# Kernel tuning notes

Hardware: AMD Instinct MI355X
Metric: run time of the kernel (lower is better)

## Reference

```python
import jax, jax.numpy as jnp
import numpy as np

D = 128   # node feature dim
C = 2     # classes
N = 50000 # nodes
E = 500000  # edges (before self-loops)
H1 = 2    # conv1 heads
NEG_SLOPE = 0.2
BN_EPS = 1e-5


def setup_inputs() -> dict:
    key = jax.random.key(0)
    ks = jax.random.split(key, 24)
    rn = lambda k, shape, s=0.05: jax.random.normal(k, shape, dtype=jnp.float32) * s
    inp = {
        'x': jax.random.normal(ks[0], (N, D), dtype=jnp.float32),
        'edge_index': jax.random.randint(ks[1], (2, E), 0, N, dtype=jnp.int64),
        # conv1: GATConv(D, D, heads=2, concat=True)
        'W1': rn(ks[2], (D, H1 * D)),
        'att_src1': rn(ks[3], (H1, D)),
        'att_dst1': rn(ks[4], (H1, D)),
        'bias1': jnp.zeros((H1 * D,), jnp.float32),
        # conv2: GATConv(2D, D, heads=1, concat=False)
        'W2': rn(ks[5], (2 * D, D)),
        'att_src2': rn(ks[6], (1, D)),
        'att_dst2': rn(ks[7], (1, D)),
        'bias2': jnp.zeros((D,), jnp.float32),
        # lin1 = MLP([3D, 96]) : Linear -> ReLU -> BatchNorm1d
        'Wl': rn(ks[8], (3 * D, 96)), 'bl': jnp.zeros((96,), jnp.float32),
        'gl': jnp.ones((96,), jnp.float32), 'betal': jnp.zeros((96,), jnp.float32),
        # mlp1 = MLP([96, 96, C]) : two (Linear -> ReLU -> BN) blocks
        'Wa': rn(ks[9], (96, 96)), 'ba': jnp.zeros((96,), jnp.float32),
        'ga': jnp.ones((96,), jnp.float32), 'betaa': jnp.zeros((96,), jnp.float32),
        'Wb': rn(ks[10], (96, C)), 'bb': jnp.zeros((C,), jnp.float32),
        'gb': jnp.ones((C,), jnp.float32), 'betab': jnp.zeros((C,), jnp.float32),
    }
    return inp


def gat_conv(x, src, dst, W, att_src, att_dst, bias, heads, out_dim, concat):
    # PyG GATConv: h = x W -> [N,H,F]; per-edge logit leakyrelu(a_s.h_src + a_d.h_dst);
    # segment softmax over edges grouped by destination; weighted scatter-sum.
    n = x.shape[0]
    h = (x @ W).reshape(n, heads, out_dim)
    a_src = jnp.einsum('nhd,hd->nh', h, att_src)  # [N,H]
    a_dst = jnp.einsum('nhd,hd->nh', h, att_dst)
    alpha = jax.nn.leaky_relu(a_src[src] + a_dst[dst], NEG_SLOPE)  # [Etot,H]
    m = jax.ops.segment_max(alpha, dst, num_segments=n)            # [N,H]
    e = jnp.exp(alpha - m[dst])
    s = jax.ops.segment_sum(e, dst, num_segments=n)
    w = e / (s[dst] + 1e-16)                                       # [Etot,H]
    out = jax.ops.segment_sum(h[src] * w[:, :, None], dst, num_segments=n)  # [N,H,F]
    out = out.reshape(n, heads * out_dim) if concat else out.mean(axis=1)
    return out + bias


def mlp_block(x, W, b, gamma, beta):
    # Linear -> ReLU -> BatchNorm1d (training-mode batch stats, biased var)
    y = jax.nn.relu(x @ W + b)
    mu = y.mean(axis=0)
    var = ((y - mu) ** 2).mean(axis=0)
    return gamma * (y - mu) / jnp.sqrt(var + BN_EPS) + beta


def reference(x, edge_index, W1, att_src1, att_dst1, bias1,
              W2, att_src2, att_dst2, bias2,
              Wl, bl, gl, betal, Wa, ba, ga, betaa, Wb, bb, gb, betab):
    n = x.shape[0]
    # PyG GATConv default add_self_loops=True
    loops = jnp.arange(n, dtype=edge_index.dtype)
    src = jnp.concatenate([edge_index[0], loops])
    dst = jnp.concatenate([edge_index[1], loops])
    x1 = gat_conv(x, src, dst, W1, att_src1, att_dst1, bias1, H1, D, True)    # [N,2D]
    x2 = gat_conv(x1, src, dst, W2, att_src2, att_dst2, bias2, 1, D, False)   # [N,D]
    h = jnp.concatenate([x1, x2], axis=1)                                      # [N,3D]
    h = mlp_block(h, Wl, bl, gl, betal)     # lin1
    h = mlp_block(h, Wa, ba, ga, betaa)     # mlp1 layer 1
    h = mlp_block(h, Wb, bb, gb, betab)     # mlp1 layer 2
    return h
```

## Files before the change

kernel.cpp:

```cpp
#include <hip/hip_runtime.h>
#include <hip/hip_bf16.h>
#include <cstdint>
#include <cstddef>

#define NNODES 50000
#define NEDGES 500000
#define ETOT   (NEDGES + NNODES)
#define MAXDEG 96

typedef __attribute__((ext_vector_type(8))) short short8;
typedef __attribute__((ext_vector_type(8))) unsigned short ushort8v;
typedef __attribute__((ext_vector_type(4))) float floatx4;
typedef __attribute__((ext_vector_type(4))) unsigned short ushort4v;

__device__ __forceinline__ unsigned short f2bf(float f) {
    union { __hip_bfloat16 h; unsigned short u; } cv;
    cv.h = __float2bfloat16(f);
    return cv.u;
}
__device__ __forceinline__ float bf2f(unsigned short u) {
    union { unsigned int i; float f; } cv;
    cv.i = ((unsigned int)u) << 16;
    return cv.f;
}

#define GBM 128
#define GBN 64
#define GBK 32

__global__ __launch_bounds__(256, 4) void gemm_mfma(
    const unsigned short* __restrict__ A, int lda,
    const unsigned short* __restrict__ Bt,
    float* __restrict__ C,
    unsigned short* __restrict__ Cb,
    const float* __restrict__ bias,
    float* __restrict__ colsum, float* __restrict__ colsq,
    const float* __restrict__ att_s, const float* __restrict__ att_d,
    float* __restrict__ as_out, float* __restrict__ ad_out, int Hheads,
    int M, int N, int K, int do_relu)
{
    __shared__ __attribute__((aligned(16))) unsigned short Alds[GBM * GBK];
    __shared__ __attribute__((aligned(16))) unsigned short Blds[GBN * GBK];
    __shared__ float scol[GBN], sqcol[GBN];

    int tid = threadIdx.x;
    int wave = tid >> 6, lane = tid & 63;
    int row0 = blockIdx.y * GBM;
    int col0 = blockIdx.x * GBN;
    int m = lane & 15, q = lane >> 4;

    floatx4 acc[2][4] = {};

    for (int k0 = 0; k0 < K; k0 += GBK) {
        #pragma unroll
        for (int i = 0; i < 2; ++i) {
            int c = tid + i * 256;
            int r = c >> 2, off = (c & 3) * 8;
            int gr = row0 + r;
            short8 v = {};
            if (gr < M) v = *(const short8*)(A + (size_t)gr * lda + k0 + off);
            *(short8*)(Alds + r * GBK + off) = v;
        }
        {
            int r = tid >> 2, off = (tid & 3) * 8;
            short8 v = *(const short8*)(Bt + (size_t)(col0 + r) * K + k0 + off);
            *(short8*)(Blds + r * GBK + off) = v;
        }
        __syncthreads();

        short8 a0 = *(const short8*)(Alds + (wave * 32 + m) * GBK + q * 8);
        short8 a1 = *(const short8*)(Alds + (wave * 32 + 16 + m) * GBK + q * 8);
        #pragma unroll
        for (int ct = 0; ct < 4; ++ct) {
            short8 b = *(const short8*)(Blds + (ct * 16 + m) * GBK + q * 8);
            acc[0][ct] = __builtin_amdgcn_mfma_f32_16x16x32_bf16(a0, b, acc[0][ct], 0, 0, 0);
            acc[1][ct] = __builtin_amdgcn_mfma_f32_16x16x32_bf16(a1, b, acc[1][ct], 0, 0, 0);
        }
        __syncthreads();
    }

    float ps[4] = {}, pq[4] = {};
    #pragma unroll
    for (int rt = 0; rt < 2; ++rt) {
        #pragma unroll
        for (int r = 0; r < 4; ++r) {
            int gr = row0 + wave * 32 + rt * 16 + q * 4 + r;
            float ds = 0.f, dd = 0.f;
            #pragma unroll
            for (int ct = 0; ct < 4; ++ct) {
                int gc = col0 + ct * 16 + m;
                float v = acc[rt][ct][r];
                if (gc < N) {
                    if (att_s != nullptr) { ds += v * att_s[gc]; dd += v * att_d[gc]; }
                    float vb = v;
                    if (bias != nullptr) vb += bias[gc];
                    if (do_relu) vb = fmaxf(vb, 0.f);
                    if (gr < M) {
                        if (C  != nullptr) C[(size_t)gr * N + gc] = vb;
                        if (Cb != nullptr) Cb[(size_t)gr * N + gc] = f2bf(vb);
                        ps[ct] += vb; pq[ct] += vb * vb;
                    }
                }
            }
            if (att_s != nullptr) {
                #pragma unroll
                for (int off = 1; off < 16; off <<= 1) {
                    ds += __shfl_xor(ds, off);
                    dd += __shfl_xor(dd, off);
                }
                if (m == 0 && gr < M) {
                    int head = col0 >> 7;
                    atomicAdd(&as_out[gr * Hheads + head], ds);
                    atomicAdd(&ad_out[gr * Hheads + head], dd);
                }
            }
        }
    }
    if (colsum != nullptr) {
        if (tid < GBN) { scol[tid] = 0.f; sqcol[tid] = 0.f; }
        __syncthreads();
        #pragma unroll
        for (int ct = 0; ct < 4; ++ct) {
            atomicAdd(&scol[ct * 16 + m], ps[ct]);
            atomicAdd(&sqcol[ct * 16 + m], pq[ct]);
        }
        __syncthreads();
        if (tid < GBN) {
            int gc = col0 + tid;
            if (gc < N) {
                atomicAdd(&colsum[gc], scol[tid]);
                atomicAdd(&colsq[gc], sqcol[tid]);
            }
        }
    }
}

__global__ void cast_x_k(const float* __restrict__ x, unsigned short* __restrict__ xb, int total4) {
    int i = blockIdx.x * blockDim.x + threadIdx.x;
    if (i >= total4) return;
    const float4 v = ((const float4*)x)[i];
    ushort4v o;
    o.x = f2bf(v.x); o.y = f2bf(v.y); o.z = f2bf(v.z); o.w = f2bf(v.w);
    ((ushort4v*)xb)[i] = o;
}

__global__ void cast_weights(const float* __restrict__ W1, const float* __restrict__ W2,
                             const float* __restrict__ Wl,
                             unsigned short* __restrict__ W1t, unsigned short* __restrict__ W2t,
                             unsigned short* __restrict__ Wlt) {
    int i = blockIdx.x * 256 + threadIdx.x;
    if (i < 32768) {
        int n = i >> 7, k = i & 127;
        W1t[i] = f2bf(W1[k * 256 + n]);
    } else if (i < 65536) {
        int j = i - 32768;
        int n = j >> 8, k = j & 255;
        W2t[j] = f2bf(W2[k * 128 + n]);
    } else if (i < 114688) {
        int j = i - 65536;
        int n = j / 384, k = j % 384;
        Wlt[j] = (n < 96) ? f2bf(Wl[(size_t)k * 96 + n]) : (unsigned short)0;
    }
}

__global__ void bnfold_a(const float* __restrict__ csum, const float* __restrict__ csq,
                         const float* __restrict__ gamma, const float* __restrict__ beta,
                         const float* __restrict__ Wa, const float* __restrict__ ba,
                         unsigned short* __restrict__ Wat2, float* __restrict__ ba_f) {
    __shared__ float scl[96], shf[96];
    int tid = threadIdx.x;
    if (tid < 96) {
        float mu  = csum[tid] / (float)NNODES;
        float var = csq[tid] / (float)NNODES - mu * mu;
        if (var < 0.f) var = 0.f;
        float sc = gamma[tid] * rsqrtf(var + 1e-5f);
        scl[tid] = sc; shf[tid] = beta[tid] - mu * sc;
    }
    __syncthreads();
    for (int idx = tid; idx < 128 * 96; idx += 256) {
        int n = idx / 96, k = idx % 96;
        Wat2[idx] = (n < 96) ? f2bf(scl[k] * Wa[k * 96 + n]) : (unsigned short)0;
    }
    if (tid < 96) {
        float s = ba[tid];
        for (int k = 0; k < 96; ++k) s += shf[k] * Wa[k * 96 + tid];
        ba_f[tid] = s;
    }
}

__global__ void bnfold_b(const float* __restrict__ csum, const float* __restrict__ csq,
                         const float* __restrict__ gamma, const float* __restrict__ beta,
                         const float* __restrict__ Wb, const float* __restrict__ bb,
                         unsigned short* __restrict__ Wbt, float* __restrict__ bb_f) {
    __shared__ float scl[96], shf[96];
    int tid = threadIdx.x;
    if (tid < 96) {
        float mu  = csum[tid] / (float)NNODES;
        float var = csq[tid] / (float)NNODES - mu * mu;
        if (var < 0.f) var = 0.f;
        float sc = gamma[tid] * rsqrtf(var + 1e-5f);
        scl[tid] = sc; shf[tid] = beta[tid] - mu * sc;
    }
    __syncthreads();
    for (int idx = tid; idx < 64 * 96; idx += 256) {
        int n = idx / 96, k = idx % 96;
        Wbt[idx] = (n < 2) ? f2bf(scl[k] * Wb[k * 2 + n]) : (unsigned short)0;
    }
    if (tid < 2) {
        float s = bb[tid];
        for (int k = 0; k < 96; ++k) s += shf[k] * Wb[k * 2 + tid];
        bb_f[tid] = s;
    }
}

__global__ void bn_fin_apply(const float* __restrict__ csum, const float* __restrict__ csq,
                             const float* __restrict__ gamma, const float* __restrict__ beta,
                             float* __restrict__ y, int total) {
    int i = blockIdx.x * blockDim.x + threadIdx.x;
    if (i >= total) return;
    int j = i & 1;
    float mu  = csum[j] / (float)NNODES;
    float var = csq[j] / (float)NNODES - mu * mu;
    if (var < 0.f) var = 0.f;
    float sc = gamma[j] * rsqrtf(var + 1e-5f);
    float sh = beta[j] - mu * sc;
    y[i] = y[i] * sc + sh;
}

__device__ __forceinline__ void edge_src_dst(const int* ei, int e, int& src, int& dst) {
    if (e < NEDGES) { src = ei[e]; dst = ei[NEDGES + e]; }
    else { src = e - NEDGES; dst = src; }
}

__global__ __launch_bounds__(256) void csr_count(const int* __restrict__ ei, int* __restrict__ cnt) {
    int e = blockIdx.x * blockDim.x + threadIdx.x;
    if (e >= ETOT) return;
    int src, dst; edge_src_dst(ei, e, src, dst); (void)src;
    atomicAdd(&cnt[dst], 1);
}

#define SCAN_CH 1024
#define SCAN_NB ((NNODES + SCAN_CH - 1) / SCAN_CH)

__global__ __launch_bounds__(256) void scan1(const int* __restrict__ cnt, int* __restrict__ part) {
    int t = threadIdx.x;
    int base = blockIdx.x * SCAN_CH + t * 4;
    int4 v = {0, 0, 0, 0};
    if (base + 3 < NNODES) v = *(const int4*)(cnt + base);
    else {
        if (base + 0 < NNODES) v.x = cnt[base + 0];
        if (base + 1 < NNODES) v.y = cnt[base + 1];
        if (base + 2 < NNODES) v.z = cnt[base + 2];
        if (base + 3 < NNODES) v.w = cnt[base + 3];
    }
    int s = v.x + v.y + v.z + v.w;
    __shared__ int sm[256];
    sm[t] = s;
    __syncthreads();
    for (int off = 128; off > 0; off >>= 1) {
        if (t < off) sm[t] += sm[t + off];
        __syncthreads();
    }
    if (t == 0) part[blockIdx.x] = sm[0];
}

__global__ void scan2(int* __restrict__ part, int* __restrict__ rowstart) {
    int lane = threadIdx.x;
    int v = (lane < SCAN_NB) ? part[lane] : 0;
    #pragma unroll
    for (int off = 1; off < 64; off <<= 1) {
        int t = __shfl_up(v, off);
        if (lane >= off) v += t;
    }
    int ex = __shfl_up(v, 1);
    if (lane == 0) ex = 0;
    if (lane < SCAN_NB) part[lane] = ex;
    if (lane == 0) rowstart[NNODES] = ETOT;
}

__global__ __launch_bounds__(256) void scan3(const int* __restrict__ cnt, const int* __restrict__ part,
                                             int* __restrict__ rowstart, int* __restrict__ cursor) {
    int t = threadIdx.x;
    int base = blockIdx.x * SCAN_CH + t * 4;
    int4 v = {0, 0, 0, 0};
    if (base + 3 < NNODES) v = *(const int4*)(cnt + base);
    else {
        if (base + 0 < NNODES) v.x = cnt[base + 0];
        if (base + 1 < NNODES) v.y = cnt[base + 1];
        if (base + 2 < NNODES) v.z = cnt[base + 2];
        if (base + 3 < NNODES) v.w = cnt[base + 3];
    }
    int s = v.x + v.y + v.z + v.w;
    __shared__ int sm[2][256];
    sm[0][t] = s;
    __syncthreads();
    int cur = 0;
    #pragma unroll
    for (int off = 1; off < 256; off <<= 1) {
        int nxt = cur ^ 1;
        int val = sm[cur][t];
        if (t >= off) val += sm[cur][t - off];
        sm[nxt][t] = val;
        __syncthreads();
        cur = nxt;
    }
    int p = sm[cur][t] - s + part[blockIdx.x];
    if (base + 0 < NNODES) { rowstart[base + 0] = p; cursor[base + 0] = p; } p += v.x;
    if (base + 1 < NNODES) { rowstart[base + 1] = p; cursor[base + 1] = p; } p += v.y;
    if (base + 2 < NNODES) { rowstart[base + 2] = p; cursor[base + 2] = p; } p += v.z;
    if (base + 3 < NNODES) { rowstart[base + 3] = p; cursor[base + 3] = p; }
}

__global__ __launch_bounds__(256) void csr_fill(const int* __restrict__ ei,
                                                int* __restrict__ cursor,
                                                int* __restrict__ esrc) {
    int e = blockIdx.x * blockDim.x + threadIdx.x;
    if (e >= ETOT) return;
    int src, dst; edge_src_dst(ei, e, src, dst);
    int pos = atomicAdd(&cursor[dst], 1);
    esrc[pos] = src;
}

__global__ __launch_bounds__(256) void gat_gather_h2(
    const int* __restrict__ rowstart, const int* __restrict__ esrc,
    const unsigned short* __restrict__ hb, const float* __restrict__ a_src,
    const float* __restrict__ a_dst, const float* __restrict__ bias,
    unsigned short* __restrict__ xcat)
{
    __shared__ float wl[4][2][MAXDEG];
    __shared__ int   esl[4][MAXDEG];
    int wave = threadIdx.x >> 6;
    int n = (blockIdx.x * blockDim.x + threadIdx.x) >> 6;
    int lane = threadIdx.x & 63;
    if (n >= NNODES) return;
    int beg = rowstart[n], end = rowstart[n + 1];
    int deg = end - beg;
    float ad0 = a_dst[n * 2], ad1 = a_dst[n * 2 + 1];

    float m0 = -1e30f, m1 = -1e30f;
    for (int idx = lane; idx < deg; idx += 64) {
        int s = esrc[beg + idx];
        float l0 = a_src[s * 2] + ad0;     l0 = l0 >= 0.f ? l0 : 0.2f * l0;
        float l1 = a_src[s * 2 + 1] + ad1; l1 = l1 >= 0.f ? l1 : 0.2f * l1;
        m0 = fmaxf(m0, l0); m1 = fmaxf(m1, l1);
        if (idx < MAXDEG) { wl[wave][0][idx] = l0; wl[wave][1][idx] = l1; esl[wave][idx] = s; }
    }
    #pragma unroll
    for (int off = 1; off < 64; off <<= 1) {
        m0 = fmaxf(m0, __shfl_xor(m0, off));
        m1 = fmaxf(m1, __shfl_xor(m1, off));
    }
    float s0 = 0.f, s1 = 0.f;
    for (int idx = lane; idx < deg; idx += 64) {
        float l0, l1;
        if (idx < MAXDEG) { l0 = wl[wave][0][idx]; l1 = wl[wave][1][idx]; }
        else {
            int s = esrc[beg + idx];
            l0 = a_src[s * 2] + ad0;     l0 = l0 >= 0.f ? l0 : 0.2f * l0;
            l1 = a_src[s * 2 + 1] + ad1; l1 = l1 >= 0.f ? l1 : 0.2f * l1;
        }
        float e0 = __expf(l0 - m0), e1 = __expf(l1 - m1);
        s0 += e0; s1 += e1;
        if (idx < MAXDEG) { wl[wave][0][idx] = e0; wl[wave][1][idx] = e1; }
    }
    #pragma unroll
    for (int off = 1; off < 64; off <<= 1) {
        s0 += __shfl_xor(s0, off);
        s1 += __shfl_xor(s1, off);
    }

    int g  = lane >> 5;
    int sl = lane & 31;
    int head = sl >> 4;
    float mh   = head ? m1 : m0;
    float invh = head ? 1.f / (s1 + 1e-16f) : 1.f / (s0 + 1e-16f);
    float adh  = head ? ad1 : ad0;

    float acc[8] = {}, acc2[8] = {};
    for (int idx = g; idx < deg; idx += 4) {
        int sA; float wA;
        if (idx < MAXDEG) { sA = esl[wave][idx]; wA = wl[wave][head][idx] * invh; }
        else {
            sA = esrc[beg + idx];
            float l = a_src[sA * 2 + head] + adh; l = l >= 0.f ? l : 0.2f * l;
            wA = __expf(l - mh) * invh;
        }
        const ushort8v hvA = *(const ushort8v*)(hb + (size_t)sA * 256 + sl * 8);
        int i2 = idx + 2;
        if (i2 < deg) {
            int sB; float wB;
            if (i2 < MAXDEG) { sB = esl[wave][i2]; wB = wl[wave][head][i2] * invh; }
            else {
                sB = esrc[beg + i2];
                float l = a_src[sB * 2 + head] + adh; l = l >= 0.f ? l : 0.2f * l;
                wB = __expf(l - mh) * invh;
            }
            const ushort8v hvB = *(const ushort8v*)(hb + (size_t)sB * 256 + sl * 8);
            #pragma unroll
            for (int j = 0; j < 8; ++j) acc2[j] += wB * bf2f(hvB[j]);
        }
        #pragma unroll
        for (int j = 0; j < 8; ++j) acc[j] += wA * bf2f(hvA[j]);
    }
    #pragma unroll
    for (int j = 0; j < 8; ++j) acc[j] += acc2[j];
    #pragma unroll
    for (int j = 0; j < 8; ++j) acc[j] += __shfl_xor(acc[j], 32);
    if (g == 0) {
        ushort8v o;
        #pragma unroll
        for (int j = 0; j < 8; ++j) o[j] = f2bf(acc[j] + bias[sl * 8 + j]);
        *(ushort8v*)(xcat + (size_t)n * 384 + sl * 8) = o;
    }
}

__global__ __launch_bounds__(256) void gat_gather_h1(
    const int* __restrict__ rowstart, const int* __restrict__ esrc,
    const unsigned short* __restrict__ hb, const float* __restrict__ a_src,
    const float* __restrict__ a_dst, const float* __restrict__ bias,
    unsigned short* __restrict__ xcat)
{
    __shared__ float wl[4][MAXDEG];
    __shared__ int   esl[4][MAXDEG];
    int wave = threadIdx.x >> 6;
    int n = (blockIdx.x * blockDim.x + threadIdx.x) >> 6;
    int lane = threadIdx.x & 63;
    if (n >= NNODES) return;
    int beg = rowstart[n], end = rowstart[n + 1];
    int deg = end - beg;
    float ad0 = a_dst[n];

    float m0 = -1e30f;
    for (int idx = lane; idx < deg; idx += 64) {
        int s = esrc[beg + idx];
        float l0 = a_src[s] + ad0; l0 = l0 >= 0.f ? l0 : 0.2f * l0;
        m0 = fmaxf(m0, l0);
        if (idx < MAXDEG) { wl[wave][idx] = l0; esl[wave][idx] = s; }
    }
    #pragma unroll
    for (int off = 1; off < 64; off <<= 1) m0 = fmaxf(m0, __shfl_xor(m0, off));
    float s0 = 0.f;
    for (int idx = lane; idx < deg; idx += 64) {
        float l0;
        if (idx < MAXDEG) l0 = wl[wave][idx];
        else {
            int s = esrc[beg + idx];
            l0 = a_src[s] + ad0; l0 = l0 >= 0.f ? l0 : 0.2f * l0;
        }
        float e0 = __expf(l0 - m0);
        s0 += e0;
        if (idx < MAXDEG) wl[wave][idx] = e0;
    }
    #pragma unroll
    for (int off = 1; off < 64; off <<= 1) s0 += __shfl_xor(s0, off);
    float inv0 = 1.f / (s0 + 1e-16f);

    int g  = lane >> 4;
    int sl = lane & 15;

    float acc[8] = {}, acc2[8] = {};
    for (int idx = g; idx < deg; idx += 8) {
        int sA; float wA;
        if (idx < MAXDEG) { sA = esl[wave][idx]; wA = wl[wave][idx] * inv0; }
        else {
            sA = esrc[beg + idx];
            float l = a_src[sA] + ad0; l = l >= 0.f ? l : 0.2f * l;
            wA = __expf(l - m0) * inv0;
        }
        const ushort8v hvA = *(const ushort8v*)(hb + (size_t)sA * 128 + sl * 8);
        int i2 = idx + 4;
        if (i2 < deg) {
            int sB; float wB;
            if (i2 < MAXDEG) { sB = esl[wave][i2]; wB = wl[wave][i2] * inv0; }
            else {
                sB = esrc[beg + i2];
                float l = a_src[sB] + ad0; l = l >= 0.f ? l : 0.2f * l;
                wB = __expf(l - m0) * inv0;
            }
            const ushort8v hvB = *(const ushort8v*)(hb + (size_t)sB * 128 + sl * 8);
            #pragma unroll
            for (int j = 0; j < 8; ++j) acc2[j] += wB * bf2f(hvB[j]);
        }
        #pragma unroll
        for (int j = 0; j < 8; ++j) acc[j] += wA * bf2f(hvA[j]);
    }
    #pragma unroll
    for (int j = 0; j < 8; ++j) acc[j] += acc2[j];
    #pragma unroll
    for (int j = 0; j < 8; ++j) acc[j] += __shfl_xor(acc[j], 16);
    #pragma unroll
    for (int j = 0; j < 8; ++j) acc[j] += __shfl_xor(acc[j], 32);
    if (g == 0) {
        ushort8v o;
        #pragma unroll
        for (int j = 0; j < 8; ++j) o[j] = f2bf(acc[j] + bias[sl * 8 + j]);
        *(ushort8v*)(xcat + (size_t)n * 384 + 256 + sl * 8) = o;
    }
}

extern "C" void kernel_launch(void* const* d_in, const int* in_sizes, int n_in,
                              void* d_out, int out_size, void* d_ws, size_t ws_size,
                              hipStream_t stream) {
    const float* x        = (const float*)d_in[0];
    const int*   ei       = (const int*)d_in[1];
    const float* W1       = (const float*)d_in[2];
    const float* att_src1 = (const float*)d_in[3];
    const float* att_dst1 = (const float*)d_in[4];
    const float* bias1    = (const float*)d_in[5];
    const float* W2       = (const float*)d_in[6];
    const float* att_src2 = (const float*)d_in[7];
    const float* att_dst2 = (const float*)d_in[8];
    const float* bias2    = (const float*)d_in[9];
    const float* Wl       = (const float*)d_in[10];
    const float* bl       = (const float*)d_in[11];
    const float* gl       = (const float*)d_in[12];
    const float* betal    = (const float*)d_in[13];
    const float* Wa       = (const float*)d_in[14];
    const float* ba       = (const float*)d_in[15];
    const float* ga       = (const float*)d_in[16];
    const float* betaa    = (const float*)d_in[17];
    const float* Wb       = (const float*)d_in[18];
    const float* bb       = (const float*)d_in[19];
    const float* gb       = (const float*)d_in[20];
    const float* betab    = (const float*)d_in[21];
    float* out = (float*)d_out;
    char* ws = (char*)d_ws;

    const int N = NNODES;

    const size_t offY2b  = 0;
    const size_t offXcat = 19200000;
    const size_t offXb   = 57600000;
    const size_t offY1b  = 70400000;
    const size_t offHb1  = 80000000;
    const size_t offW1t  = 105600000;
    const size_t offW2t  = 105665536;
    const size_t offWlt  = 105731072;
    const size_t offWat2 = 105829376;
    const size_t offWbt  = 105853952;
    const size_t offBaf  = 105866240;
    const size_t offBbf  = 105866640;
    const size_t offRow  = 106000000;
    const size_t offCur  = 106200128;
    const size_t offEsrc = 106400832;
    const size_t offPart = 108700000;
    const size_t offAs1  = 108800000;
    const size_t offAd1  = 109200000;
    const size_t offAs2  = 109600000;
    const size_t offAd2  = 109800000;
    const size_t offSt   = 110000000;

    unsigned short* y2b  = (unsigned short*)(ws + offY2b);
    unsigned short* xcat = (unsigned short*)(ws + offXcat);
    unsigned short* xb   = (unsigned short*)(ws + offXb);
    unsigned short* hb2  = (unsigned short*)(ws + offXb);
    unsigned short* y1b  = (unsigned short*)(ws + offY1b);
    unsigned short* hb1  = (unsigned short*)(ws + offHb1);
    unsigned short* W1t  = (unsigned short*)(ws + offW1t);
    unsigned short* W2t  = (unsigned short*)(ws + offW2t);
    unsigned short* Wlt  = (unsigned short*)(ws + offWlt);
    unsigned short* Wat2 = (unsigned short*)(ws + offWat2);
    unsigned short* Wbt  = (unsigned short*)(ws + offWbt);
    float* ba_f = (float*)(ws + offBaf);
    float* bb_f = (float*)(ws + offBbf);
    int* rowst  = (int*)(ws + offRow);
    int* cursor = (int*)(ws + offCur);
    int* esrc   = (int*)(ws + offEsrc);
    int* part   = (int*)(ws + offPart);
    float* as1  = (float*)(ws + offAs1);
    float* ad1  = (float*)(ws + offAd1);
    float* as2  = (float*)(ws + offAs2);
    float* ad2  = (float*)(ws + offAd2);

    float* csum_l = (float*)(ws + offSt + 0);
    float* csq_l  = (float*)(ws + offSt + 512);
    float* csum_a = (float*)(ws + offSt + 2048);
    float* csq_a  = (float*)(ws + offSt + 2560);
    float* csum_b = (float*)(ws + offSt + 4096);
    float* csq_b  = (float*)(ws + offSt + 4608);

    hipMemsetAsync(ws + offRow, 0, (NNODES + 1) * sizeof(int), stream);
    hipMemsetAsync(ws + offAs1, 0, (offSt + 6144) - offAs1, stream);

    dim3 blk(256);
    int edgeBlocks  = (ETOT + 255) / 256;
    int waveBlocksN = (N + 3) / 4;

    cast_x_k<<<(N * 128 / 4 + 255) / 256, blk, 0, stream>>>(x, xb, N * 128 / 4);
    cast_weights<<<(114688 + 255) / 256, blk, 0, stream>>>(W1, W2, Wl, W1t, W2t, Wlt);

    csr_count<<<edgeBlocks, blk, 0, stream>>>(ei, rowst);
    scan1<<<SCAN_NB, blk, 0, stream>>>(rowst, part);
    scan2<<<1, 64, 0, stream>>>(part, rowst);
    scan3<<<SCAN_NB, blk, 0, stream>>>(rowst, part, rowst, cursor);
    csr_fill<<<edgeBlocks, blk, 0, stream>>>(ei, cursor, esrc);

    gemm_mfma<<<dim3(4, (N + GBM - 1) / GBM), blk, 0, stream>>>(
        xb, 128, W1t, nullptr, hb1, nullptr, nullptr, nullptr,
        att_src1, att_dst1, as1, ad1, 2, N, 256, 128, 0);
    gat_gather_h2<<<waveBlocksN, blk, 0, stream>>>(rowst, esrc, hb1, as1, ad1, bias1, xcat);

    gemm_mfma<<<dim3(2, (N + GBM - 1) / GBM), blk, 0, stream>>>(
        xcat, 384, W2t, nullptr, hb2, nullptr, nullptr, nullptr,
        att_src2, att_dst2, as2, ad2, 1, N, 128, 256, 0);
    gat_gather_h1<<<waveBlocksN, blk, 0, stream>>>(rowst, esrc, hb2, as2, ad2, bias2, xcat);

    gemm_mfma<<<dim3(2, (N + GBM - 1) / GBM), blk, 0, stream>>>(
        xcat, 384, Wlt, nullptr, y1b, bl, csum_l, csq_l,
        nullptr, nullptr, nullptr, nullptr, 0, N, 96, 384, 1);
    bnfold_a<<<1, 256, 0, stream>>>(csum_l, csq_l, gl, betal, Wa, ba, Wat2, ba_f);

    gemm_mfma<<<dim3(2, (N + GBM - 1) / GBM), blk, 0, stream>>>(
        y1b, 96, Wat2, nullptr, y2b, ba_f, csum_a, csq_a,
        nullptr, nullptr, nullptr, nullptr, 0, N, 96, 96, 1);
    bnfold_b<<<1, 256, 0, stream>>>(csum_a, csq_a, ga, betaa, Wb, bb, Wbt, bb_f);

    gemm_mfma<<<dim3(1, (N + GBM - 1) / GBM), blk, 0, stream>>>(
        y2b, 96, Wbt, out, nullptr, bb_f, csum_b, csq_b,
        nullptr, nullptr, nullptr, nullptr, 0, N, 2, 96, 1);

    bn_fin_apply<<<(N * 2 + 255) / 256, blk, 0, stream>>>(csum_b, csq_b, gb, betab, out, N * 2);
}
```

Before: 400.8 us.

## Aggregate raw features before conv1 projection and fold attention vectors into weights

Conv1 now gathers neighbours of the 128-wide bf16 input x with per-head softmax weights, then applies W1 per head with two GEMMs. Before, the 256-wide projected h was gathered. Attention logits for conv1 come from precomputed U1 = W1·att vectors, applied in the cast kernel. Conv2 logits come from U2 folded into the first-layer GEMM epilogue, which now applies them after bias. The goal is to halve gather bytes per edge and drop the first full projection GEMM, at the cost of two per-head GEMMs and extra small kernels.

```diff
diff --git a/kernel.cpp b/kernel.cpp
--- a/kernel.cpp
+++ b/kernel.cpp
@@ -32,7 +32,7 @@
     const unsigned short* __restrict__ A, int lda,
     const unsigned short* __restrict__ Bt,
     float* __restrict__ C,
-    unsigned short* __restrict__ Cb,
+    unsigned short* __restrict__ Cb, int ldc,
     const float* __restrict__ bias,
     float* __restrict__ colsum, float* __restrict__ colsq,
     const float* __restrict__ att_s, const float* __restrict__ att_d,
@@ -91,13 +91,13 @@
                 int gc = col0 + ct * 16 + m;
                 float v = acc[rt][ct][r];
                 if (gc < N) {
-                    if (att_s != nullptr) { ds += v * att_s[gc]; dd += v * att_d[gc]; }
                     float vb = v;
                     if (bias != nullptr) vb += bias[gc];
                     if (do_relu) vb = fmaxf(vb, 0.f);
+                    if (att_s != nullptr) { ds += vb * att_s[gc]; dd += vb * att_d[gc]; }
                     if (gr < M) {
-                        if (C  != nullptr) C[(size_t)gr * N + gc] = vb;
-                        if (Cb != nullptr) Cb[(size_t)gr * N + gc] = f2bf(vb);
+                        if (C  != nullptr) C[(size_t)gr * ldc + gc] = vb;
+                        if (Cb != nullptr) Cb[(size_t)gr * ldc + gc] = f2bf(vb);
                         ps[ct] += vb; pq[ct] += vb * vb;
                     }
                 }
@@ -135,13 +135,77 @@
     }
 }
 
-__global__ void cast_x_k(const float* __restrict__ x, unsigned short* __restrict__ xb, int total4) {
-    int i = blockIdx.x * blockDim.x + threadIdx.x;
-    if (i >= total4) return;
-    const float4 v = ((const float4*)x)[i];
+__global__ __launch_bounds__(256) void fold_att(
+    const float* __restrict__ W1, const float* __restrict__ as1v, const float* __restrict__ ad1v,
+    const float* __restrict__ W2, const float* __restrict__ as2v, const float* __restrict__ ad2v,
+    float* __restrict__ U1, float* __restrict__ U2)
+{
+    int g = threadIdx.x >> 5, l = threadIdx.x & 31;
+    int task = blockIdx.x * 8 + g;
+    float ss = 0.f, sd = 0.f;
+    if (task < 256) {
+        int d = task & 127, h = task >> 7;
+        const float4 wv = *(const float4*)(W1 + d * 256 + h * 128 + l * 4);
+        const float4 av = *(const float4*)(as1v + h * 128 + l * 4);
+        const float4 bv = *(const float4*)(ad1v + h * 128 + l * 4);
+        ss = wv.x * av.x + wv.y * av.y + wv.z * av.z + wv.w * av.w;
+        sd = wv.x * bv.x + wv.y * bv.y + wv.z * bv.z + wv.w * bv.w;
+    } else {
+        int k = task - 256;
+        const float4 wv = *(const float4*)(W2 + (size_t)k * 128 + l * 4);
+        const float4 av = *(const float4*)(as2v + l * 4);
+        const float4 bv = *(const float4*)(ad2v + l * 4);
+        ss = wv.x * av.x + wv.y * av.y + wv.z * av.z + wv.w * av.w;
+        sd = wv.x * bv.x + wv.y * bv.y + wv.z * bv.z + wv.w * bv.w;
+    }
+    #pragma unroll
+    for (int off = 1; off < 32; off <<= 1) { ss += __shfl_xor(ss, off); sd += __shfl_xor(sd, off); }
+    if (l == 0) {
+        if (task < 256) {
+            int d = task & 127, h = task >> 7;
+            U1[h * 128 + d] = ss;
+            U1[256 + h * 128 + d] = sd;
+        } else {
+            int k = task - 256;
+            U2[k] = ss;
+            U2[256 + k] = sd;
+        }
+    }
+}
+
+__global__ __launch_bounds__(256) void cast_x_att(
+    const float* __restrict__ x, const float* __restrict__ U1,
+    unsigned short* __restrict__ xb, float* __restrict__ as1, float* __restrict__ ad1)
+{
+    __shared__ float Us[512];
+    int tid = threadIdx.x;
+    Us[tid] = U1[tid];
+    Us[tid + 256] = U1[tid + 256];
+    __syncthreads();
+    int g = tid >> 5, l = tid & 31;
+    int n = blockIdx.x * 8 + g;
+    if (n >= NNODES) return;
+    const float4 v = *(const float4*)(x + (size_t)n * 128 + l * 4);
     ushort4v o;
     o.x = f2bf(v.x); o.y = f2bf(v.y); o.z = f2bf(v.z); o.w = f2bf(v.w);
-    ((ushort4v*)xb)[i] = o;
+    *(ushort4v*)(xb + (size_t)n * 128 + l * 4) = o;
+    const float4 us0 = *(const float4*)(Us + l * 4);
+    const float4 us1 = *(const float4*)(Us + 128 + l * 4);
+    const float4 ud0 = *(const float4*)(Us + 256 + l * 4);
+    const float4 ud1 = *(const float4*)(Us + 384 + l * 4);
+    float s0 = v.x * us0.x + v.y * us0.y + v.z * us0.z + v.w * us0.w;
+    float s1 = v.x * us1.x + v.y * us1.y + v.z * us1.z + v.w * us1.w;
+    float d0 = v.x * ud0.x + v.y * ud0.y + v.z * ud0.z + v.w * ud0.w;
+    float d1 = v.x * ud1.x + v.y * ud1.y + v.z * ud1.z + v.w * ud1.w;
+    #pragma unroll
+    for (int off = 1; off < 32; off <<= 1) {
+        s0 += __shfl_xor(s0, off); s1 += __shfl_xor(s1, off);
+        d0 += __shfl_xor(d0, off); d1 += __shfl_xor(d1, off);
+    }
+    if (l == 0) {
+        as1[n * 2] = s0; as1[n * 2 + 1] = s1;
+        ad1[n * 2] = d0; ad1[n * 2 + 1] = d1;
+    }
 }
 
 __global__ void cast_weights(const float* __restrict__ W1, const float* __restrict__ W2,
@@ -321,11 +385,10 @@
     esrc[pos] = src;
 }
 
-__global__ __launch_bounds__(256) void gat_gather_h2(
+__global__ __launch_bounds__(256) void gat_gather_x2(
     const int* __restrict__ rowstart, const int* __restrict__ esrc,
-    const unsigned short* __restrict__ hb, const float* __restrict__ a_src,
-    const float* __restrict__ a_dst, const float* __restrict__ bias,
-    unsigned short* __restrict__ xcat)
+    const unsigned short* __restrict__ xb, const float* __restrict__ a_src,
+    const float* __restrict__ a_dst, unsigned short* __restrict__ xaggh)
 {
     __shared__ float wl[4][2][MAXDEG];
     __shared__ int   esl[4][MAXDEG];
@@ -368,49 +431,62 @@
         s0 += __shfl_xor(s0, off);
         s1 += __shfl_xor(s1, off);
     }
-
-    int g  = lane >> 5;
-    int sl = lane & 31;
-    int head = sl >> 4;
-    float mh   = head ? m1 : m0;
-    float invh = head ? 1.f / (s1 + 1e-16f) : 1.f / (s0 + 1e-16f);
-    float adh  = head ? ad1 : ad0;
-
-    float acc[8] = {}, acc2[8] = {};
-    for (int idx = g; idx < deg; idx += 4) {
-        int sA; float wA;
-        if (idx < MAXDEG) { sA = esl[wave][idx]; wA = wl[wave][head][idx] * invh; }
-        else {
+    float inv0 = 1.f / (s0 + 1e-16f), inv1 = 1.f / (s1 + 1e-16f);
+
+    int g  = lane >> 4;
+    int sl = lane & 15;
+
+    float a0[8] = {}, a1[8] = {}, b0[8] = {}, b1[8] = {};
+    for (int idx = g; idx < deg; idx += 8) {
+        int sA; float wA0, wA1;
+        if (idx < MAXDEG) {
+            sA = esl[wave][idx];
+            wA0 = wl[wave][0][idx] * inv0; wA1 = wl[wave][1][idx] * inv1;
+        } else {
             sA = esrc[beg + idx];
-            float l = a_src[sA * 2 + head] + adh; l = l >= 0.f ? l : 0.2f * l;
-            wA = __expf(l - mh) * invh;
-        }
-        const ushort8v hvA = *(const ushort8v*)(hb + (size_t)sA * 256 + sl * 8);
-        int i2 = idx + 2;
+            float l0 = a_src[sA * 2] + ad0;     l0 = l0 >= 0.f ? l0 : 0.2f * l0;
+            float l1 = a_src[sA * 2 + 1] + ad1; l1 = l1 >= 0.f ? l1 : 0.2f * l1;
+            wA0 = __expf(l0 - m0) * inv0; wA1 = __expf(l1 - m1) * inv1;
+        }
+        const ushort8v hvA = *(const ushort8v*)(xb + (size_t)sA * 128 + sl * 8);
+        int i2 = idx + 4;
         if (i2 < deg) {
-            int sB; float wB;
-            if (i2 < MAXDEG) { sB = esl[wave][i2]; wB = wl[wave][head][i2] * invh; }
-            else {
+            int sB; float wB0, wB1;
+            if (i2 < MAXDEG) {
+                sB = esl[wave][i2];
+                wB0 = wl[wave][0][i2] * inv0; wB1 = wl[wave][1][i2] * inv1;
+            } else {
                 sB = esrc[beg + i2];
-                float l = a_src[sB * 2 + head] + adh; l = l >= 0.f ? l : 0.2f * l;
-                wB = __expf(l - mh) * invh;
+                float l0 = a_src[sB * 2] + ad0;     l0 = l0 >= 0.f ? l0 : 0.2f * l0;
+                float l1 = a_src[sB * 2 + 1] + ad1; l1 = l1 >= 0.f ? l1 : 0.2f * l1;
+                wB0 = __expf(l0 - m0) * inv0; wB1 = __expf(l1 - m1) * inv1;
             }
-            const ushort8v hvB = *(const ushort8v*)(hb + (size_t)sB * 256 + sl * 8);
+            const ushort8v hvB = *(const ushort8v*)(xb + (size_t)sB * 128 + sl * 8);
             #pragma unroll
-            for (int j = 0; j < 8; ++j) acc2[j] += wB * bf2f(hvB[j]);
+            for (int j = 0; j < 8; ++j) {
+                float f = bf2f(hvB[j]);
+                b0[j] += wB0 * f; b1[j] += wB1 * f;
+            }
         }
         #pragma unroll
-        for (int j = 0; j < 8; ++j) acc[j] += wA * bf2f(hvA[j]);
-    }
-    #pragma unroll
-    for (int j = 0; j < 8; ++j) acc[j] += acc2[j];
-    #pragma unroll
-    for (int j = 0; j < 8; ++j) acc[j] += __shfl_xor(acc[j], 32);
+        for (int j = 0; j < 8; ++j) {
+            float f = bf2f(hvA[j]);
+            a0[j] += wA0 * f; a1[j] += wA1 * f;
+        }
+    }
+    #pragma unroll
+    for (int j = 0; j < 8; ++j) { a0[j] += b0[j]; a1[j] += b1[j]; }
+    #pragma unroll
+    for (int j = 0; j < 8; ++j) {
+        a0[j] += __shfl_xor(a0[j], 16); a0[j] += __shfl_xor(a0[j], 32);
+        a1[j] += __shfl_xor(a1[j], 16); a1[j] += __shfl_xor(a1[j], 32);
+    }
     if (g == 0) {
-        ushort8v o;
+        ushort8v o0, o1;
         #pragma unroll
-        for (int j = 0; j < 8; ++j) o[j] = f2bf(acc[j] + bias[sl * 8 + j]);
-        *(ushort8v*)(xcat + (size_t)n * 384 + sl * 8) = o;
+        for (int j = 0; j < 8; ++j) { o0[j] = f2bf(a0[j]); o1[j] = f2bf(a1[j]); }
+        *(ushort8v*)(xaggh + (size_t)n * 256 + sl * 8) = o0;
+        *(ushort8v*)(xaggh + (size_t)n * 256 + 128 + sl * 8) = o1;
     }
 }
 
@@ -532,7 +608,7 @@
     const size_t offXcat = 19200000;
     const size_t offXb   = 57600000;
     const size_t offY1b  = 70400000;
-    const size_t offHb1  = 80000000;
+    const size_t offXagg = 80000000;
     const size_t offW1t  = 105600000;
     const size_t offW2t  = 105665536;
     const size_t offWlt  = 105731072;
@@ -540,6 +616,8 @@
     const size_t offWbt  = 105853952;
     const size_t offBaf  = 105866240;
     const size_t offBbf  = 105866640;
+    const size_t offU1   = 105867264;
+    const size_t offU2   = 105869312;
     const size_t offRow  = 106000000;
     const size_t offCur  = 106200128;
     const size_t offEsrc = 106400832;
@@ -550,19 +628,21 @@
     const size_t offAd2  = 109800000;
     const size_t offSt   = 110000000;
 
-    unsigned short* y2b  = (unsigned short*)(ws + offY2b);
-    unsigned short* xcat = (unsigned short*)(ws + offXcat);
-    unsigned short* xb   = (unsigned short*)(ws + offXb);
-    unsigned short* hb2  = (unsigned short*)(ws + offXb);
-    unsigned short* y1b  = (unsigned short*)(ws + offY1b);
-    unsigned short* hb1  = (unsigned short*)(ws + offHb1);
-    unsigned short* W1t  = (unsigned short*)(ws + offW1t);
-    unsigned short* W2t  = (unsigned short*)(ws + offW2t);
-    unsigned short* Wlt  = (unsigned short*)(ws + offWlt);
-    unsigned short* Wat2 = (unsigned short*)(ws + offWat2);
-    unsigned short* Wbt  = (unsigned short*)(ws + offWbt);
+    unsigned short* y2b   = (unsigned short*)(ws + offY2b);
+    unsigned short* xcat  = (unsigned short*)(ws + offXcat);
+    unsigned short* xb    = (unsigned short*)(ws + offXb);
+    unsigned short* hb2   = (unsigned short*)(ws + offXb);
+    unsigned short* y1b   = (unsigned short*)(ws + offY1b);
+    unsigned short* xaggh = (unsigned short*)(ws + offXagg);
+    unsigned short* W1t   = (unsigned short*)(ws + offW1t);
+    unsigned short* W2t   = (unsigned short*)(ws + offW2t);
+    unsigned short* Wlt   = (unsigned short*)(ws + offWlt);
+    unsigned short* Wat2  = (unsigned short*)(ws + offWat2);
+    unsigned short* Wbt   = (unsigned short*)(ws + offWbt);
     float* ba_f = (float*)(ws + offBaf);
     float* bb_f = (float*)(ws + offBbf);
+    float* U1   = (float*)(ws + offU1);
+    float* U2   = (float*)(ws + offU2);
     int* rowst  = (int*)(ws + offRow);
     int* cursor = (int*)(ws + offCur);
     int* esrc   = (int*)(ws + offEsrc);
@@ -585,8 +665,10 @@
     dim3 blk(256);
     int edgeBlocks  = (ETOT + 255) / 256;
     int waveBlocksN = (N + 3) / 4;
-
-    cast_x_k<<<(N * 128 / 4 + 255) / 256, blk, 0, stream>>>(x, xb, N * 128 / 4);
+    dim3 gemmRows((N + GBM - 1) / GBM);
+
+    fold_att<<<64, blk, 0, stream>>>(W1, att_src1, att_dst1, W2, att_src2, att_dst2, U1, U2);
+    cast_x_att<<<(N + 7) / 8, blk, 0, stream>>>(x, U1, xb, as1, ad1);
     cast_weights<<<(114688 + 255) / 256, blk, 0, stream>>>(W1, W2, Wl, W1t, W2t, Wlt);
 
     csr_count<<<edgeBlocks, blk, 0, stream>>>(ei, rowst);
@@ -595,28 +677,31 @@
     scan3<<<SCAN_NB, blk, 0, stream>>>(rowst, part, rowst, cursor);
     csr_fill<<<edgeBlocks, blk, 0, stream>>>(ei, cursor, esrc);
 
-    gemm_mfma<<<dim3(4, (N + GBM - 1) / GBM), blk, 0, stream>>>(
-        xb, 128, W1t, nullptr, hb1, nullptr, nullptr, nullptr,
-        att_src1, att_dst1, as1, ad1, 2, N, 256, 128, 0);
-    gat_gather_h2<<<waveBlocksN, blk, 0, stream>>>(rowst, esrc, hb1, as1, ad1, bias1, xcat);
-
-    gemm_mfma<<<dim3(2, (N + GBM - 1) / GBM), blk, 0, stream>>>(
-        xcat, 384, W2t, nullptr, hb2, nullptr, nullptr, nullptr,
-        att_src2, att_dst2, as2, ad2, 1, N, 128, 256, 0);
+    gat_gather_x2<<<waveBlocksN, blk, 0, stream>>>(rowst, esrc, xb, as1, ad1, xaggh);
+    gemm_mfma<<<dim3(2, gemmRows.x), blk, 0, stream>>>(
+        xaggh, 256, W1t, nullptr, xcat, 384, bias1, nullptr, nullptr,
+        U2, U2 + 256, as2, ad2, 1, N, 128, 128, 0);
+    gemm_mfma<<<dim3(2, gemmRows.x), blk, 0, stream>>>(
+        xaggh + 128, 256, W1t + 128 * 128, nullptr, xcat + 128, 384, bias1 + 128,
+        nullptr, nullptr, U2 + 128, U2 + 384, as2, ad2, 1, N, 128, 128, 0);
+
+    gemm_mfma<<<dim3(2, gemmRows.x), blk, 0, stream>>>(
+        xcat, 384, W2t, nullptr, hb2, 128, nullptr, nullptr, nullptr,
+        nullptr, nullptr, nullptr, nullptr, 0, N, 128, 256, 0);
     gat_gather_h1<<<waveBlocksN, blk, 0, stream>>>(rowst, esrc, hb2, as2, ad2, bias2, xcat);
 
-    gemm_mfma<<<dim3(2, (N + GBM - 1) / GBM), blk, 0, stream>>>(
-        xcat, 384, Wlt, nullptr, y1b, bl, csum_l, csq_l,
+    gemm_mfma<<<dim3(2, gemmRows.x), blk, 0, stream>>>(
+        xcat, 384, Wlt, nullptr, y1b, 96, bl, csum_l, csq_l,
         nullptr, nullptr, nullptr, nullptr, 0, N, 96, 384, 1);
     bnfold_a<<<1, 256, 0, stream>>>(csum_l, csq_l, gl, betal, Wa, ba, Wat2, ba_f);
 
-    gemm_mfma<<<dim3(2, (N + GBM - 1) / GBM), blk, 0, stream>>>(
-        y1b, 96, Wat2, nullptr, y2b, ba_f, csum_a, csq_a,
+    gemm_mfma<<<dim3(2, gemmRows.x), blk, 0, stream>>>(
+        y1b, 96, Wat2, nullptr, y2b, 96, ba_f, csum_a, csq_a,
         nullptr, nullptr, nullptr, nullptr, 0, N, 96, 96, 1);
     bnfold_b<<<1, 256, 0, stream>>>(csum_a, csq_a, ga, betaa, Wb, bb, Wbt, bb_f);
 
-    gemm_mfma<<<dim3(1, (N + GBM - 1) / GBM), blk, 0, stream>>>(
-        y2b, 96, Wbt, out, nullptr, bb_f, csum_b, csq_b,
+    gemm_mfma<<<dim3(1, gemmRows.x), blk, 0, stream>>>(
+        y2b, 96, Wbt, out, nullptr, 2, bb_f, csum_b, csq_b,
         nullptr, nullptr, nullptr, nullptr, 0, N, 2, 96, 1);
 
     bn_fin_apply<<<(N * 2 + 255) / 256, blk, 0, stream>>>(csum_b, csq_b, gb, betab, out, N * 2);
```

New measurement: 410.9 us. 2.5% more time.
